# Kernel optimization log

Measured on AMD Instinct MI355X. Metric: run time of the kernel, lower is better.

The kernel has to match this reference:

```python
import jax, jax.numpy as jnp
import numpy as np

NUM_HEADS = 8
HEAD_SPLITS = [2, 3, 3]   # heads per conv window group (windows 3,5,7)


def _dwconv(x, w, b):
    # depthwise conv2d, SAME padding; x [B,Cg,H,W], w [Cg,1,k,k]
    k = w.shape[-1]
    pad = k // 2
    out = jax.lax.conv_general_dilated(
        x, w, window_strides=(1, 1), padding=[(pad, pad), (pad, pad)],
        feature_group_count=x.shape[1])
    return out + b[None, :, None, None]


def setup_inputs() -> dict:
    key = jax.random.key(0)
    ks = jax.random.split(key, 8)
    B, Hs, Ws, C = 16, 56, 56, 512
    N = 1 + Hs * Ws
    Ch = C // NUM_HEADS
    inp = {
        "x": jax.random.normal(ks[0], (B, N, C), dtype=jnp.float32),
        "qkv_w": jax.random.normal(ks[1], (3 * C, C), dtype=jnp.float32) * 0.02,
        "qkv_b": jnp.zeros((3 * C,), dtype=jnp.float32),
        "proj_w": jax.random.normal(ks[2], (C, C), dtype=jnp.float32) * 0.02,
        "proj_b": jnp.zeros((C,), dtype=jnp.float32),
        "conv_w3": jax.random.normal(ks[3], (2 * Ch, 1, 3, 3), dtype=jnp.float32) * 0.1,
        "conv_b3": jnp.zeros((2 * Ch,), dtype=jnp.float32),
        "conv_w5": jax.random.normal(ks[4], (3 * Ch, 1, 5, 5), dtype=jnp.float32) * 0.1,
        "conv_b5": jnp.zeros((3 * Ch,), dtype=jnp.float32),
        "conv_w7": jax.random.normal(ks[5], (3 * Ch, 1, 7, 7), dtype=jnp.float32) * 0.1,
        "conv_b7": jnp.zeros((3 * Ch,), dtype=jnp.float32),
        "H": 56,
        "W": 56,
    }
    return inp


def reference(x, qkv_w, qkv_b, proj_w, proj_b,
              conv_w3, conv_b3, conv_w5, conv_b5, conv_w7, conv_b7, H, W):
    B, N, C = x.shape
    h = NUM_HEADS
    Ch = C // h
    scale = Ch ** -0.5

    # qkv projection -> [3, B, h, N, Ch]
    qkv = (x @ qkv_w.T + qkv_b).reshape(B, N, 3, h, Ch)
    qkv = jnp.transpose(qkv, (2, 0, 3, 1, 4))
    q, k, v = qkv[0], qkv[1], qkv[2]

    # linear-attention factorization: softmax over tokens, then small Ch x Ch matmuls
    k_sm = jax.nn.softmax(k, axis=2)                     # softmax over N
    kv = jnp.einsum('bhnk,bhnd->bhkd', k_sm, v)          # [B,h,Ch,Ch]
    factor_att = jnp.einsum('bhnk,bhkd->bhnd', q, kv)    # [B,h,N,Ch]

    # conv relative-position encoding (CoaT ConvRelPosEnc)
    q_img = q[:, :, 1:, :]                               # drop CLS token
    v_img = v[:, :, 1:, :]
    v_img = jnp.transpose(v_img, (0, 1, 3, 2)).reshape(B, h * Ch, H, W)
    splits = np.cumsum([s * Ch for s in HEAD_SPLITS])[:-1]
    p3, p5, p7 = jnp.split(v_img, splits, axis=1)
    conv_v = jnp.concatenate([
        _dwconv(p3, conv_w3, conv_b3),
        _dwconv(p5, conv_w5, conv_b5),
        _dwconv(p7, conv_w7, conv_b7)], axis=1)           # [B,h*Ch,H,W]
    conv_v = jnp.transpose(conv_v.reshape(B, h, Ch, H * W), (0, 1, 3, 2))
    ev = q_img * conv_v                                   # [B,h,HW,Ch]
    crpe = jnp.concatenate(
        [jnp.zeros((B, h, 1, Ch), dtype=x.dtype), ev], axis=2)

    out = scale * factor_att + crpe                       # [B,h,N,Ch]
    out = jnp.transpose(out, (0, 2, 1, 3)).reshape(B, N, C)
    return out @ proj_w.T + proj_b
```

## Files before the change

kernel.cpp:

```cpp
#include <hip/hip_runtime.h>
#include <stdint.h>

#define NHEADS 8
#define NTOK   3137
#define BATCH  16
#define CDIM   512
#define MT     (BATCH*NTOK)

typedef unsigned short u16;
typedef float f32x4  __attribute__((ext_vector_type(4)));
typedef short bf16x8 __attribute__((ext_vector_type(8)));

__device__ __forceinline__ float bf2f(u16 u){
  union { uint32_t i; float f; } x; x.i = ((uint32_t)u) << 16; return x.f;
}
__device__ __forceinline__ u16 f2bf(float f){
  union { float f; uint32_t i; } x; x.f = f;
  uint32_t r = x.i + 0x7fffu + ((x.i >> 16) & 1u);
  return (u16)(r >> 16);
}
__device__ __forceinline__ void async_ld16(void* lds, const void* g){
  __builtin_amdgcn_global_load_lds((const __attribute__((address_space(1))) void*)g,
                                   (__attribute__((address_space(3))) void*)lds, 16, 0, 0);
}
#define BARM()   asm volatile("s_barrier" ::: "memory")
#define WAITV(N) asm volatile("s_waitcnt vmcnt(" #N ")" ::: "memory")
#define MFMA16(d,a,b) d = __builtin_amdgcn_mfma_f32_16x16x32_bf16(a,b,d,0,0,0)

__global__ void cvt_kernel(const float* __restrict__ src, u16* __restrict__ dst, int n4){
  int i = blockIdx.x * blockDim.x + threadIdx.x;
  if (i < n4){
    float4 v = ((const float4*)src)[i];
    uint32_t lo = ((uint32_t)f2bf(v.y) << 16) | f2bf(v.x);
    uint32_t hi = ((uint32_t)f2bf(v.w) << 16) | f2bf(v.z);
    ((uint2*)dst)[i] = make_uint2(lo, hi);
  }
}

template<int BM,int BN,int WM,int WN,int MODE>
__global__ __launch_bounds__(WM*WN*64, 2) void gemm2(
    const u16* __restrict__ A, const u16* __restrict__ Bw, const float* __restrict__ bias,
    u16* __restrict__ q_s, u16* __restrict__ k_s, u16* __restrict__ v_s,
    float* __restrict__ outF, int M)
{
  constexpr int THREADS = WM*WN*64;
  constexpr int MF = BM/(WM*16);
  constexpr int NF = BN/(WN*16);
  constexpr int WROWS = BM/WM;
  constexpr int WCOLS = BN/WN;
  static_assert((BM*8)/THREADS + (BN*8)/THREADS == 8, "vmcnt literal assumes 8 loads/stage");
  __shared__ __align__(16) u16 smem[2*(BM+BN)*64];

  const int t = threadIdx.x;
  const int w = t >> 6, l = t & 63;
  const int wr = w / WN, wc = w % WN;
  const int lr = l & 15, lg = l >> 4;

  const int nx = gridDim.x;
  const int nwg = nx * gridDim.y;
  const int orig = blockIdx.y * nx + blockIdx.x;
  const int q8 = nwg >> 3, r8 = nwg & 7;
  const int xcd = orig & 7;
  const int wgid = (xcd < r8 ? xcd*(q8+1) : r8*(q8+1) + (xcd-r8)*q8) + (orig >> 3);
  const int n0 = (wgid % nx) * BN;
  const int m0 = (wgid / nx) * BM;

  f32x4 acc[MF][NF];
#pragma unroll
  for (int i=0;i<MF;i++)
#pragma unroll
    for (int j=0;j<NF;j++) acc[i][j] = (f32x4){0.f,0.f,0.f,0.f};

  auto stage = [&](int bi, int k0){
    u16* da = smem + bi*(BM*64);
    u16* db = smem + 2*BM*64 + bi*(BN*64);
#pragma unroll
    for (int j=0;j<(BM*8)/THREADS;j++){
      int qc = t + THREADS*j;
      int R = qc >> 3, c = qc & 7;
      int cs = (c ^ (R & 7)) * 8;
      int ar = m0 + R; if (ar > M-1) ar = M-1;
      async_ld16(&da[qc*8], &A[(size_t)ar*512 + k0 + cs]);
    }
#pragma unroll
    for (int j=0;j<(BN*8)/THREADS;j++){
      int qc = t + THREADS*j;
      int R = qc >> 3, c = qc & 7;
      int cs = (c ^ (R & 7)) * 8;
      async_ld16(&db[qc*8], &Bw[(size_t)(n0+R)*512 + k0 + cs]);
    }
  };

  stage(0, 0);
  int cur = 0;
  for (int kt = 0; kt < 8; ++kt){
    if (kt < 7) stage(cur ^ 1, (kt+1)*64);
    if (kt < 7) { WAITV(8); } else { WAITV(0); }
    BARM();
    const u16* a_base = smem + cur*(BM*64);
    const u16* b_base = smem + 2*BM*64 + cur*(BN*64);
    __builtin_amdgcn_s_setprio(1);
#pragma unroll
    for (int ks=0; ks<2; ks++){
      bf16x8 af[MF], bfv[NF];
      int chunk = ks*4 + lg;
#pragma unroll
      for (int fi=0;fi<MF;fi++){
        int row = wr*WROWS + fi*16 + lr;
        af[fi] = *(const bf16x8*)&a_base[row*64 + ((chunk ^ (row & 7))*8)];
      }
#pragma unroll
      for (int fj=0;fj<NF;fj++){
        int col = wc*WCOLS + fj*16 + lr;
        bfv[fj] = *(const bf16x8*)&b_base[col*64 + ((chunk ^ (col & 7))*8)];
      }
#pragma unroll
      for (int fi=0;fi<MF;fi++)
#pragma unroll
        for (int fj=0;fj<NF;fj++)
          acc[fi][fj] = __builtin_amdgcn_mfma_f32_16x16x32_bf16(af[fi], bfv[fj], acc[fi][fj], 0, 0, 0);
    }
    __builtin_amdgcn_s_setprio(0);
    BARM();
    cur ^= 1;
  }

  if (MODE == 0){
    u16* warea = smem + w * (WROWS*WCOLS);
    float bvv[NF];
#pragma unroll
    for (int fj=0;fj<NF;fj++) bvv[fj] = bias[n0 + wc*WCOLS + fj*16 + lr];
#pragma unroll
    for (int fi=0;fi<MF;fi++)
#pragma unroll
      for (int fj=0;fj<NF;fj++)
#pragma unroll
        for (int r=0;r<4;r++)
          warea[(fi*16 + lg*4 + r)*WCOLS + fj*16 + lr] = f2bf(acc[fi][fj][r] + bvv[fj]);
    __syncthreads();
    const int colo = n0 + wc*WCOLS;
    const int part = colo >> 9;
    const int hq   = (colo >> 6) & 7;
    u16* dst = (part == 0) ? q_s : ((part == 1) ? k_s : v_s);
    const int rsub = l >> 3;
    const int csub = (l & 7) * 8;
#pragma unroll
    for (int pass=0; pass<WROWS/8; ++pass){
      int rl = pass*8 + rsub;
      int m = m0 + wr*WROWS + rl;
      if (m < M){
        int bb = m / NTOK;
        int n  = m - bb*NTOK;
        uint4 vv = *(const uint4*)&warea[rl*WCOLS + csub];
        *(uint4*)&dst[((size_t)(bb*8 + hq)*NTOK + n)*64 + csub] = vv;
      }
    }
  } else {
    float* warea = (float*)smem + w * (WROWS*WCOLS);
    float bvv[NF];
#pragma unroll
    for (int fj=0;fj<NF;fj++) bvv[fj] = bias[n0 + wc*WCOLS + fj*16 + lr];
#pragma unroll
    for (int fi=0;fi<MF;fi++)
#pragma unroll
      for (int fj=0;fj<NF;fj++)
#pragma unroll
        for (int r=0;r<4;r++)
          warea[(fi*16 + lg*4 + r)*WCOLS + fj*16 + lr] = acc[fi][fj][r] + bvv[fj];
    __syncthreads();
    const int colo = n0 + wc*WCOLS;
    const int rsub = l >> 4;
    const int csub = (l & 15) * 4;
#pragma unroll
    for (int pass=0; pass<WROWS/4; ++pass){
      int rl = pass*4 + rsub;
      int m = m0 + wr*WROWS + rl;
      if (m < M){
        float4 vv = *(const float4*)&warea[rl*WCOLS + csub];
        *(float4*)&outF[(size_t)m*512 + colo + csub] = vv;
      }
    }
  }
}

__global__ __launch_bounds__(256) void kv_partial(
    const u16* __restrict__ k_s, const u16* __restrict__ v_s,
    float* __restrict__ kv_p, float* __restrict__ s_p)
{
  __shared__ float smem[18432];
  const int t  = threadIdx.x;
  const int bh = blockIdx.x;
  const int hf = blockIdx.y;
  const size_t base = (size_t)bh * NTOK * 64;
  const int srow = t >> 3;
  const int scol = (t & 7) * 8;
  const int ns = t >> 6;
  const int kg = (t >> 3) & 7;
  const int dg = t & 7;

  float accv[8][8];
#pragma unroll
  for (int a=0;a<8;a++)
#pragma unroll
    for (int c=0;c<8;c++) accv[a][c] = 0.f;
  float s_loc[8];
#pragma unroll
  for (int i=0;i<8;i++) s_loc[i] = 0.f;

  float* ek = smem;
  float* vv = smem + 2048;
  const int n_beg = hf * 800;
  const int n_end = (hf == 3) ? NTOK : (n_beg + 800);

  for (int n0 = n_beg; n0 < n_end; n0 += 32){
    __syncthreads();
    int n = n0 + srow;
    float et[8], vf[8];
    if (n < n_end){
      uint4 kvec = *(const uint4*)&k_s[base + (size_t)n*64 + scol];
      uint4 vvec = *(const uint4*)&v_s[base + (size_t)n*64 + scol];
      const u16* kp = (const u16*)&kvec;
      const u16* vp = (const u16*)&vvec;
#pragma unroll
      for (int i=0;i<8;i++){
        et[i] = __expf(bf2f(kp[i]));
        s_loc[i] += et[i];
        vf[i] = bf2f(vp[i]);
      }
    } else {
#pragma unroll
      for (int i=0;i<8;i++){ et[i]=0.f; vf[i]=0.f; }
    }
    *(float4*)&ek[srow*64 + scol]     = make_float4(et[0],et[1],et[2],et[3]);
    *(float4*)&ek[srow*64 + scol + 4] = make_float4(et[4],et[5],et[6],et[7]);
    *(float4*)&vv[srow*64 + scol]     = make_float4(vf[0],vf[1],vf[2],vf[3]);
    *(float4*)&vv[srow*64 + scol + 4] = make_float4(vf[4],vf[5],vf[6],vf[7]);
    __syncthreads();
#pragma unroll
    for (int i=0;i<8;i++){
      int nl = ns + 4*i;
      float4 e0 = *(const float4*)&ek[nl*64 + kg*8];
      float4 e1 = *(const float4*)&ek[nl*64 + kg*8 + 4];
      float4 v0 = *(const float4*)&vv[nl*64 + dg*8];
      float4 v1 = *(const float4*)&vv[nl*64 + dg*8 + 4];
      float ea[8] = {e0.x,e0.y,e0.z,e0.w,e1.x,e1.y,e1.z,e1.w};
      float va[8] = {v0.x,v0.y,v0.z,v0.w,v1.x,v1.y,v1.z,v1.w};
#pragma unroll
      for (int a=0;a<8;a++)
#pragma unroll
        for (int c=0;c<8;c++) accv[a][c] += ea[a]*va[c];
    }
  }
  __syncthreads();
  float* part_kv = smem;
  float* part_s  = smem + 16384;
#pragma unroll
  for (int a=0;a<8;a++)
#pragma unroll
    for (int c=0;c<8;c++)
      part_kv[(size_t)ns*4096 + (kg*8+a)*64 + dg*8+c] = accv[a][c];
#pragma unroll
  for (int i=0;i<8;i++) part_s[srow*64 + scol + i] = s_loc[i];
  __syncthreads();
  const size_t obase = ((size_t)hf*128 + bh) * 4096;
  for (int i=0;i<16;i++){
    int e = t*16 + i;
    kv_p[obase + e] = part_kv[e] + part_kv[4096+e] + part_kv[8192+e] + part_kv[12288+e];
  }
  if (t < 64){
    float s = 0.f;
    for (int r=0;r<32;r++) s += part_s[r*64 + t];
    s_p[((size_t)hf*128 + bh)*64 + t] = s;
  }
}

__global__ void kv_reduce(const float* __restrict__ kv_p, const float* __restrict__ s_p,
                          u16* __restrict__ kvT){
  const int bh = blockIdx.x, t = threadIdx.x;
  for (int i=0;i<16;i++){
    int e = t*16 + i;
    int k = e >> 6, d = e & 63;
    float v = 0.f, S = 0.f;
#pragma unroll
    for (int hf=0; hf<4; hf++){
      v += kv_p[(size_t)(hf*128 + bh)*4096 + e];
      S += s_p[(hf*128 + bh)*64 + k];
    }
    kvT[(size_t)bh*4096 + d*64 + k] = f2bf(v / S);
  }
}

template<int R>
__global__ __launch_bounds__(256) void conv_fa(
    const u16* __restrict__ v_s, const u16* __restrict__ q_s,
    const u16* __restrict__ kvT,
    const float* __restrict__ wsrc, const float* __restrict__ bsrc,
    int h0, u16* __restrict__ out_pre)
{
  constexpr int KK = 2*R + 1;
  constexpr int TAPS = KK*KK;
  __shared__ __align__(16) u16 smem[8192 + KK*3584];
  u16* vt = smem + 8192;
  const int t = threadIdx.x;
  const int y  = blockIdx.x;
  const int hh = blockIdx.y;
  const int b  = blockIdx.z;
  const int h  = h0 + hh;
  const int bh = b*8 + h;
  const size_t base = (size_t)bh * NTOK * 64;
  const int n0 = 1 + y*56;

#pragma unroll
  for (int j=0;j<2;j++){
    int qq = t + 256*j;
    int row = qq >> 3, c = qq & 7;
    int cs = (c ^ (row & 7)) * 8;
    int n = n0 + row; if (n > NTOK-1) n = NTOK-1;
    async_ld16(&smem[qq*8], &q_s[base + (size_t)n*64 + cs]);
    async_ld16(&smem[4096 + qq*8], &kvT[(size_t)bh*4096 + row*64 + cs]);
  }
  for (int ry=0; ry<KK; ry++){
    int yy = y - R + ry;
    for (int idx = t; idx < 448; idx += 256){
      uint4 val = make_uint4(0u,0u,0u,0u);
      if (yy >= 0 && yy < 56)
        val = *(const uint4*)&v_s[base + (size_t)(1 + yy*56)*64 + idx*8];
      *(uint4*)&vt[ry*3584 + idx*8] = val;
    }
  }
  __syncthreads();

  const int w = t >> 6, l = t & 63;
  const int lr = l & 15, lg = l >> 4;
  f32x4 fac[4];
#pragma unroll
  for (int j=0;j<4;j++) fac[j] = (f32x4){0.f,0.f,0.f,0.f};
#pragma unroll
  for (int ks=0; ks<2; ks++){
    int chunk = ks*4 + lg;
    int arow = w*16 + lr;
    bf16x8 af = *(const bf16x8*)&smem[arow*64 + ((chunk ^ (arow & 7))*8)];
#pragma unroll
    for (int fj=0; fj<4; fj++){
      int col = fj*16 + lr;
      bf16x8 bvv = *(const bf16x8*)&smem[4096 + col*64 + ((chunk ^ (col & 7))*8)];
      MFMA16(fac[fj], af, bvv);
    }
  }

  const int d = l;
  const int xg = w;
  float wreg[TAPS];
#pragma unroll
  for (int i=0;i<TAPS;i++) wreg[i] = wsrc[(hh*64 + d)*TAPS + i];
  const float bias = bsrc[hh*64 + d];
  float creg[14];
#pragma unroll
  for (int i=0;i<14;i++) creg[i] = bias;
  const int x0 = xg * 14;
#pragma unroll
  for (int ry=0; ry<KK; ry++){
    float rw[14 + 2*R];
#pragma unroll
    for (int i=0; i<14+2*R; i++){
      int xx = x0 - R + i;
      rw[i] = (xx >= 0 && xx < 56) ? bf2f(vt[ry*3584 + xx*64 + d]) : 0.f;
    }
#pragma unroll
    for (int xi=0; xi<14; xi++)
#pragma unroll
      for (int rx=0; rx<KK; rx++)
        creg[xi] += rw[xi+rx] * wreg[ry*KK + rx];
  }

  float qv[14];
#pragma unroll
  for (int xi=0; xi<14; xi++){
    int row = x0 + xi;
    int chunk = d >> 3, e = d & 7;
    qv[xi] = bf2f(smem[row*64 + ((chunk ^ (row & 7))*8) + e]);
  }

  __syncthreads();
  float* fa = (float*)smem;
#pragma unroll
  for (int fj=0; fj<4; fj++)
#pragma unroll
    for (int r=0; r<4; r++)
      fa[(w*16 + lg*4 + r)*64 + fj*16 + lr] = 0.125f * fac[fj][r];
  __syncthreads();

#pragma unroll
  for (int xi=0; xi<14; xi++){
    int nn = n0 + x0 + xi;
    out_pre[((size_t)b*NTOK + nn)*CDIM + h*64 + d] =
        f2bf(fa[(x0 + xi)*64 + d] + creg[xi]*qv[xi]);
  }
}

__global__ void fa0_kernel(const u16* __restrict__ q_s, const u16* __restrict__ kvT,
                           u16* __restrict__ out_pre){
  const int b = blockIdx.x, t = threadIdx.x;
  const int h = t >> 6, d = t & 63;
  const int bh = b*8 + h;
  float s = 0.f;
#pragma unroll
  for (int k=0; k<64; k++)
    s += bf2f(q_s[(size_t)bh*NTOK*64 + k]) * bf2f(kvT[(size_t)bh*4096 + d*64 + k]);
  out_pre[(size_t)b*NTOK*CDIM + h*64 + d] = f2bf(0.125f * s);
}

extern "C" void kernel_launch(void* const* d_in, const int* in_sizes, int n_in,
                              void* d_out, int out_size, void* d_ws, size_t ws_size,
                              hipStream_t stream)
{
  const float* x      = (const float*)d_in[0];
  const float* qkv_w  = (const float*)d_in[1];
  const float* qkv_b  = (const float*)d_in[2];
  const float* proj_w = (const float*)d_in[3];
  const float* proj_b = (const float*)d_in[4];
  const float* w3 = (const float*)d_in[5];
  const float* b3 = (const float*)d_in[6];
  const float* w5 = (const float*)d_in[7];
  const float* b5 = (const float*)d_in[8];
  const float* w7 = (const float*)d_in[9];
  const float* b7 = (const float*)d_in[10];
  float* out = (float*)d_out;

  char* ws = (char*)d_ws;
  size_t off = 0;
  auto alloc = [&](size_t bytes) -> void* {
    void* p = ws + off;
    off += (bytes + 255) & ~(size_t)255;
    return p;
  };
  u16*   x_bf     = (u16*)alloc((size_t)MT*512*2);
  u16*   qkvw_bf  = (u16*)alloc((size_t)1536*512*2);
  u16*   projw_bf = (u16*)alloc((size_t)512*512*2);
  u16*   q_s      = (u16*)alloc((size_t)128*NTOK*64*2);
  u16*   k_s      = (u16*)alloc((size_t)128*NTOK*64*2);
  u16*   v_s      = (u16*)alloc((size_t)128*NTOK*64*2);
  u16*   kvT      = (u16*)alloc((size_t)128*4096*2);
  float* kv_p     = (float*)alloc((size_t)4*128*4096*4);
  float* s_p      = (float*)alloc((size_t)4*128*64*4);
  u16*   out_pre  = x_bf;

  { int n4 = (MT*512)/4;   cvt_kernel<<<(n4+255)/256, 256, 0, stream>>>(x, x_bf, n4); }
  { int n4 = (1536*512)/4; cvt_kernel<<<(n4+255)/256, 256, 0, stream>>>(qkv_w, qkvw_bf, n4); }
  { int n4 = (512*512)/4;  cvt_kernel<<<(n4+255)/256, 256, 0, stream>>>(proj_w, projw_bf, n4); }

  gemm2<256,256,2,4,0><<<dim3(6, 197), 512, 0, stream>>>(
      x_bf, qkvw_bf, qkv_b, q_s, k_s, v_s, nullptr, MT);

  kv_partial<<<dim3(128, 4), 256, 0, stream>>>(k_s, v_s, kv_p, s_p);
  kv_reduce<<<128, 256, 0, stream>>>(kv_p, s_p, kvT);
  fa0_kernel<<<16, 512, 0, stream>>>(q_s, kvT, out_pre);

  conv_fa<1><<<dim3(56, 2, 16), 256, 0, stream>>>(v_s, q_s, kvT, w3, b3, 0, out_pre);
  conv_fa<2><<<dim3(56, 3, 16), 256, 0, stream>>>(v_s, q_s, kvT, w5, b5, 2, out_pre);
  conv_fa<3><<<dim3(56, 3, 16), 256, 0, stream>>>(v_s, q_s, kvT, w7, b7, 5, out_pre);

  gemm2<128,128,2,2,1><<<dim3(4, 393), 256, 0, stream>>>(
      out_pre, projw_bf, proj_b, nullptr, nullptr, nullptr, out, MT);
}
```

Before: 383.9 us.

## Drop GEMM double buffering and raise occupancy target with halved LDS

The bf16 MFMA GEMM loses its double-buffered LDS pipeline: each k-step now loads into a single buffer, waits for all loads, then computes. The launch-bounds minimum-blocks hint goes from 2 to 4, and the epilogue is split into two half-tile passes so the staging area fits in the smaller LDS. The aim is to hide memory latency with more resident workgroups instead of software prefetching. The price is no overlap of loads and compute within a block, plus heavy register pressure: the 256x256 tile keeps 128 accumulator floats per thread, which may spill under the tighter register budget.

Measured after the change: 973.4 us. +153.5%, slower.

```diff
diff --git a/kernel.cpp b/kernel.cpp
--- a/kernel.cpp
+++ b/kernel.cpp
@@ -38,7 +38,7 @@
 }
 
 template<int BM,int BN,int WM,int WN,int MODE>
-__global__ __launch_bounds__(WM*WN*64, 2) void gemm2(
+__global__ __launch_bounds__(WM*WN*64, 4) void gemmS(
     const u16* __restrict__ A, const u16* __restrict__ Bw, const float* __restrict__ bias,
     u16* __restrict__ q_s, u16* __restrict__ k_s, u16* __restrict__ v_s,
     float* __restrict__ outF, int M)
@@ -48,8 +48,7 @@
   constexpr int NF = BN/(WN*16);
   constexpr int WROWS = BM/WM;
   constexpr int WCOLS = BN/WN;
-  static_assert((BM*8)/THREADS + (BN*8)/THREADS == 8, "vmcnt literal assumes 8 loads/stage");
-  __shared__ __align__(16) u16 smem[2*(BM+BN)*64];
+  __shared__ __align__(16) u16 smem[(BM+BN)*64];
 
   const int t = threadIdx.x;
   const int w = t >> 6, l = t & 63;
@@ -71,9 +70,11 @@
 #pragma unroll
     for (int j=0;j<NF;j++) acc[i][j] = (f32x4){0.f,0.f,0.f,0.f};
 
-  auto stage = [&](int bi, int k0){
-    u16* da = smem + bi*(BM*64);
-    u16* db = smem + 2*BM*64 + bi*(BN*64);
+  u16* da = smem;
+  u16* db = smem + BM*64;
+
+  for (int kt = 0; kt < 8; ++kt){
+    const int k0 = kt*64;
 #pragma unroll
     for (int j=0;j<(BM*8)/THREADS;j++){
       int qc = t + THREADS*j;
@@ -89,16 +90,8 @@
       int cs = (c ^ (R & 7)) * 8;
       async_ld16(&db[qc*8], &Bw[(size_t)(n0+R)*512 + k0 + cs]);
     }
-  };
-
-  stage(0, 0);
-  int cur = 0;
-  for (int kt = 0; kt < 8; ++kt){
-    if (kt < 7) stage(cur ^ 1, (kt+1)*64);
-    if (kt < 7) { WAITV(8); } else { WAITV(0); }
+    WAITV(0);
     BARM();
-    const u16* a_base = smem + cur*(BM*64);
-    const u16* b_base = smem + 2*BM*64 + cur*(BN*64);
     __builtin_amdgcn_s_setprio(1);
 #pragma unroll
     for (int ks=0; ks<2; ks++){
@@ -107,12 +100,12 @@
 #pragma unroll
       for (int fi=0;fi<MF;fi++){
         int row = wr*WROWS + fi*16 + lr;
-        af[fi] = *(const bf16x8*)&a_base[row*64 + ((chunk ^ (row & 7))*8)];
+        af[fi] = *(const bf16x8*)&da[row*64 + ((chunk ^ (row & 7))*8)];
       }
 #pragma unroll
       for (int fj=0;fj<NF;fj++){
         int col = wc*WCOLS + fj*16 + lr;
-        bfv[fj] = *(const bf16x8*)&b_base[col*64 + ((chunk ^ (col & 7))*8)];
+        bfv[fj] = *(const bf16x8*)&db[col*64 + ((chunk ^ (col & 7))*8)];
       }
 #pragma unroll
       for (int fi=0;fi<MF;fi++)
@@ -122,22 +115,15 @@
     }
     __builtin_amdgcn_s_setprio(0);
     BARM();
-    cur ^= 1;
-  }
+  }
+
+  float bvv[NF];
+#pragma unroll
+  for (int fj=0;fj<NF;fj++) bvv[fj] = bias[n0 + wc*WCOLS + fj*16 + lr];
 
   if (MODE == 0){
-    u16* warea = smem + w * (WROWS*WCOLS);
-    float bvv[NF];
-#pragma unroll
-    for (int fj=0;fj<NF;fj++) bvv[fj] = bias[n0 + wc*WCOLS + fj*16 + lr];
-#pragma unroll
-    for (int fi=0;fi<MF;fi++)
-#pragma unroll
-      for (int fj=0;fj<NF;fj++)
-#pragma unroll
-        for (int r=0;r<4;r++)
-          warea[(fi*16 + lg*4 + r)*WCOLS + fj*16 + lr] = f2bf(acc[fi][fj][r] + bvv[fj]);
-    __syncthreads();
+    constexpr int PR = WROWS/2;
+    u16* warea = smem + w * (PR*WCOLS);
     const int colo = n0 + wc*WCOLS;
     const int part = colo >> 9;
     const int hq   = (colo >> 6) & 7;
@@ -145,39 +131,53 @@
     const int rsub = l >> 3;
     const int csub = (l & 7) * 8;
 #pragma unroll
-    for (int pass=0; pass<WROWS/8; ++pass){
-      int rl = pass*8 + rsub;
-      int m = m0 + wr*WROWS + rl;
-      if (m < M){
-        int bb = m / NTOK;
-        int n  = m - bb*NTOK;
-        uint4 vv = *(const uint4*)&warea[rl*WCOLS + csub];
-        *(uint4*)&dst[((size_t)(bb*8 + hq)*NTOK + n)*64 + csub] = vv;
+    for (int p=0; p<2; ++p){
+#pragma unroll
+      for (int fh=0; fh<MF/2; fh++){
+        int fi = p*(MF/2) + fh;
+#pragma unroll
+        for (int fj=0;fj<NF;fj++)
+#pragma unroll
+          for (int r=0;r<4;r++)
+            warea[(fh*16 + lg*4 + r)*WCOLS + fj*16 + lr] = f2bf(acc[fi][fj][r] + bvv[fj]);
+      }
+#pragma unroll
+      for (int pass=0; pass<PR/8; ++pass){
+        int rl = pass*8 + rsub;
+        int m = m0 + wr*WROWS + p*PR + rl;
+        if (m < M){
+          int bb = m / NTOK;
+          int n  = m - bb*NTOK;
+          uint4 vv = *(const uint4*)&warea[rl*WCOLS + csub];
+          *(uint4*)&dst[((size_t)(bb*8 + hq)*NTOK + n)*64 + csub] = vv;
+        }
       }
     }
   } else {
-    float* warea = (float*)smem + w * (WROWS*WCOLS);
-    float bvv[NF];
-#pragma unroll
-    for (int fj=0;fj<NF;fj++) bvv[fj] = bias[n0 + wc*WCOLS + fj*16 + lr];
-#pragma unroll
-    for (int fi=0;fi<MF;fi++)
-#pragma unroll
-      for (int fj=0;fj<NF;fj++)
-#pragma unroll
-        for (int r=0;r<4;r++)
-          warea[(fi*16 + lg*4 + r)*WCOLS + fj*16 + lr] = acc[fi][fj][r] + bvv[fj];
-    __syncthreads();
+    constexpr int PR = WROWS/2;
+    float* warea = (float*)smem + w * (PR*WCOLS);
     const int colo = n0 + wc*WCOLS;
     const int rsub = l >> 4;
     const int csub = (l & 15) * 4;
 #pragma unroll
-    for (int pass=0; pass<WROWS/4; ++pass){
-      int rl = pass*4 + rsub;
-      int m = m0 + wr*WROWS + rl;
-      if (m < M){
-        float4 vv = *(const float4*)&warea[rl*WCOLS + csub];
-        *(float4*)&outF[(size_t)m*512 + colo + csub] = vv;
+    for (int p=0; p<2; ++p){
+#pragma unroll
+      for (int fh=0; fh<MF/2; fh++){
+        int fi = p*(MF/2) + fh;
+#pragma unroll
+        for (int fj=0;fj<NF;fj++)
+#pragma unroll
+          for (int r=0;r<4;r++)
+            warea[(fh*16 + lg*4 + r)*WCOLS + fj*16 + lr] = acc[fi][fj][r] + bvv[fj];
+      }
+#pragma unroll
+      for (int pass=0; pass<PR/4; ++pass){
+        int rl = pass*4 + rsub;
+        int m = m0 + wr*WROWS + p*PR + rl;
+        if (m < M){
+          float4 vv = *(const float4*)&warea[rl*WCOLS + csub];
+          *(float4*)&outF[(size_t)m*512 + colo + csub] = vv;
+        }
       }
     }
   }
@@ -449,7 +449,7 @@
   { int n4 = (1536*512)/4; cvt_kernel<<<(n4+255)/256, 256, 0, stream>>>(qkv_w, qkvw_bf, n4); }
   { int n4 = (512*512)/4;  cvt_kernel<<<(n4+255)/256, 256, 0, stream>>>(proj_w, projw_bf, n4); }
 
-  gemm2<256,256,2,4,0><<<dim3(6, 197), 512, 0, stream>>>(
+  gemmS<256,256,2,4,0><<<dim3(6, 197), 512, 0, stream>>>(
       x_bf, qkvw_bf, qkv_b, q_s, k_s, v_s, nullptr, MT);
 
   kv_partial<<<dim3(128, 4), 256, 0, stream>>>(k_s, v_s, kv_p, s_p);
@@ -460,6 +460,6 @@
   conv_fa<2><<<dim3(56, 3, 16), 256, 0, stream>>>(v_s, q_s, kvT, w5, b5, 2, out_pre);
   conv_fa<3><<<dim3(56, 3, 16), 256, 0, stream>>>(v_s, q_s, kvT, w7, b7, 5, out_pre);
 
-  gemm2<128,128,2,2,1><<<dim3(4, 393), 256, 0, stream>>>(
+  gemmS<128,128,2,2,1><<<dim3(4, 393), 256, 0, stream>>>(
       out_pre, projw_bf, proj_b, nullptr, nullptr, nullptr, out, MT);
 }
```
